# Kernel tuning notes

Measured on AMD Instinct MI355X. Metric: run time of the kernel, lower is better.

The kernel has to match this reference:

```python
import jax, jax.numpy as jnp
import numpy as np
import math

B, T, C = 8, 2048, 1024
N_LAYER, LAYER_ID = 24, 12


def setup_inputs() -> dict:
    key = jax.random.key(0)
    ks = jax.random.split(key, 8)
    # deterministic parameter init, mirroring RWKV_TimeMix.__init__
    ratio_0_to_1 = LAYER_ID / (N_LAYER - 1)
    ratio_1_to_almost0 = 1.0 - LAYER_ID / N_LAYER
    h = np.arange(C, dtype=np.float64)
    time_decay = (-5 + 8 * (h / (C - 1)) ** (0.7 + 1.3 * ratio_0_to_1)).astype(np.float32)
    zigzag = (np.array([(i + 1) % 3 - 1 for i in range(C)], dtype=np.float64) * 0.5)
    time_first = (np.ones(C) * math.log(0.3) + zigzag).astype(np.float32)
    xpos = (np.arange(C, dtype=np.float64) / C)
    time_mix_k = (xpos ** ratio_1_to_almost0).astype(np.float32).reshape(1, 1, C)
    time_mix_v = (xpos ** ratio_1_to_almost0 + 0.3 * ratio_0_to_1).astype(np.float32).reshape(1, 1, C)
    time_mix_r = (xpos ** (0.5 * ratio_1_to_almost0)).astype(np.float32).reshape(1, 1, C)
    scale = 1.0 / math.sqrt(C)
    return {
        "x": jax.random.normal(ks[0], (B, T, C), jnp.float32),
        "time_decay": jnp.asarray(time_decay),
        "time_first": jnp.asarray(time_first),
        "time_mix_k": jnp.asarray(time_mix_k),
        "time_mix_v": jnp.asarray(time_mix_v),
        "time_mix_r": jnp.asarray(time_mix_r),
        "Wk": jax.random.normal(ks[1], (C, C), jnp.float32) * scale,
        "Wv": jax.random.normal(ks[2], (C, C), jnp.float32) * scale,
        "Wr": jax.random.normal(ks[3], (C, C), jnp.float32) * scale,
        "Wo": jax.random.normal(ks[4], (C, C), jnp.float32) * scale,
    }


def wkv_scan(w_decay, u, k, v):
    """Numerically-stable RWKV-4 WKV recurrence.
    w_decay, u: [C]; k, v: [B, T, C]. Returns [B, T, C].
    """
    w = -jnp.exp(w_decay)  # negative decay per channel
    kt = jnp.swapaxes(k, 0, 1)  # [T, B, C]
    vt = jnp.swapaxes(v, 0, 1)
    Bn, Cn = k.shape[0], k.shape[2]
    aa0 = jnp.zeros((Bn, Cn), k.dtype)
    bb0 = jnp.zeros((Bn, Cn), k.dtype)
    pp0 = jnp.full((Bn, Cn), -1e38, k.dtype)

    def step(carry, kv):
        aa, bb, pp = carry
        k_t, v_t = kv
        ww = u + k_t
        q = jnp.maximum(pp, ww)
        e1 = jnp.exp(pp - q)
        e2 = jnp.exp(ww - q)
        y = (e1 * aa + e2 * v_t) / (e1 * bb + e2)
        ww2 = pp + w
        q2 = jnp.maximum(ww2, k_t)
        e1 = jnp.exp(ww2 - q2)
        e2 = jnp.exp(k_t - q2)
        return (e1 * aa + e2 * v_t, e1 * bb + e2, q2), y

    _, ys = jax.lax.scan(step, (aa0, bb0, pp0), (kt, vt))
    return jnp.swapaxes(ys, 0, 1)  # [B, T, C]


def reference(x, time_decay, time_first, time_mix_k, time_mix_v, time_mix_r, Wk, Wv, Wr, Wo):
    # time shift: x_{t-1}, zero at t=0
    xx = jnp.pad(x, ((0, 0), (1, 0), (0, 0)))[:, :-1]
    xk = x * time_mix_k + xx * (1.0 - time_mix_k)
    xv = x * time_mix_v + xx * (1.0 - time_mix_v)
    xr = x * time_mix_r + xx * (1.0 - time_mix_r)
    k = jnp.einsum("btc,oc->bto", xk, Wk)
    v = jnp.einsum("btc,oc->bto", xv, Wv)
    r = jnp.einsum("btc,oc->bto", xr, Wr)
    wkv = wkv_scan(time_decay, time_first, k, v)
    rwkv = jax.nn.sigmoid(r) * wkv
    return jnp.einsum("btc,oc->bto", rwkv, Wo)
```

## Files before the change

kernel.cpp:

```cpp
#include <hip/hip_runtime.h>

#define BB 8
#define TT 2048
#define CC 1024
#define WKV_L 32
#define WKV_NCH (TT / WKV_L)
#define WKV_LOG_NCH 6

typedef __bf16 bf16x8_t __attribute__((ext_vector_type(8)));
typedef float f32x4_t __attribute__((ext_vector_type(4)));
typedef unsigned short ushort8_t __attribute__((ext_vector_type(8)));

__device__ __forceinline__ unsigned short f2bf(float f) {
  unsigned u = __float_as_uint(f);
  u += 0x7fffu + ((u >> 16) & 1u);
  return (unsigned short)(u >> 16);
}
__device__ __forceinline__ float bf2f(unsigned short s) {
  return __uint_as_float(((unsigned)s) << 16);
}

#define GLOAD16(gp, lp)                                                        \
  __builtin_amdgcn_global_load_lds(                                            \
      (const __attribute__((address_space(1))) void*)(gp),                     \
      (__attribute__((address_space(3))) void*)(lp), 16, 0, 0)

#define MIXGRID 2048
#define CASTGRID 256

__global__ __launch_bounds__(256) void mix3_castw_kernel(
    const float* __restrict__ x, const float* __restrict__ tmk,
    const float* __restrict__ tmv, const float* __restrict__ tmr,
    unsigned short* __restrict__ xk, unsigned short* __restrict__ xv,
    unsigned short* __restrict__ xr,
    const float* __restrict__ w0, const float* __restrict__ w1,
    const float* __restrict__ w2, const float* __restrict__ w3,
    unsigned short* __restrict__ o0, unsigned short* __restrict__ o1,
    unsigned short* __restrict__ o2, unsigned short* __restrict__ o3) {
  const int bid = blockIdx.x;
  const int tid = threadIdx.x;
  if (bid < MIXGRID) {
    const size_t total8 = (size_t)BB * TT * CC / 8;
    for (size_t i = (size_t)bid * 256 + tid; i < total8;
         i += (size_t)MIXGRID * 256) {
      size_t e = i * 8;
      int c = (int)(e & (CC - 1));
      int t = (int)((e >> 10) & (TT - 1));
      float4 xa = *(const float4*)(x + e);
      float4 xb = *(const float4*)(x + e + 4);
      float4 pa = make_float4(0.f, 0.f, 0.f, 0.f), pb = pa;
      if (t > 0) {
        pa = *(const float4*)(x + e - CC);
        pb = *(const float4*)(x + e - CC + 4);
      }
      float4 mka = *(const float4*)(tmk + c), mkb = *(const float4*)(tmk + c + 4);
      float4 mva = *(const float4*)(tmv + c), mvb = *(const float4*)(tmv + c + 4);
      float4 mra = *(const float4*)(tmr + c), mrb = *(const float4*)(tmr + c + 4);
      ushort8_t ok, ov, orr;
#define MIX1(dst, idx, xv_, pv_, m_) dst[idx] = f2bf(xv_ * m_ + pv_ * (1.f - m_));
      MIX1(ok, 0, xa.x, pa.x, mka.x) MIX1(ok, 1, xa.y, pa.y, mka.y)
      MIX1(ok, 2, xa.z, pa.z, mka.z) MIX1(ok, 3, xa.w, pa.w, mka.w)
      MIX1(ok, 4, xb.x, pb.x, mkb.x) MIX1(ok, 5, xb.y, pb.y, mkb.y)
      MIX1(ok, 6, xb.z, pb.z, mkb.z) MIX1(ok, 7, xb.w, pb.w, mkb.w)
      MIX1(ov, 0, xa.x, pa.x, mva.x) MIX1(ov, 1, xa.y, pa.y, mva.y)
      MIX1(ov, 2, xa.z, pa.z, mva.z) MIX1(ov, 3, xa.w, pa.w, mva.w)
      MIX1(ov, 4, xb.x, pb.x, mvb.x) MIX1(ov, 5, xb.y, pb.y, mvb.y)
      MIX1(ov, 6, xb.z, pb.z, mvb.z) MIX1(ov, 7, xb.w, pb.w, mvb.w)
      MIX1(orr, 0, xa.x, pa.x, mra.x) MIX1(orr, 1, xa.y, pa.y, mra.y)
      MIX1(orr, 2, xa.z, pa.z, mra.z) MIX1(orr, 3, xa.w, pa.w, mra.w)
      MIX1(orr, 4, xb.x, pb.x, mrb.x) MIX1(orr, 5, xb.y, pb.y, mrb.y)
      MIX1(orr, 6, xb.z, pb.z, mrb.z) MIX1(orr, 7, xb.w, pb.w, mrb.w)
#undef MIX1
      *(ushort8_t*)(xk + e) = ok;
      *(ushort8_t*)(xv + e) = ov;
      *(ushort8_t*)(xr + e) = orr;
    }
  } else {
    const int n4 = CC * CC / 4;
    for (int i = (bid - MIXGRID) * 256 + tid; i < 4 * n4;
         i += CASTGRID * 256) {
      int sel = i / n4;
      int j = i - sel * n4;
      const float* w = sel == 0 ? w0 : sel == 1 ? w1 : sel == 2 ? w2 : w3;
      unsigned short* o = sel == 0 ? o0 : sel == 1 ? o1 : sel == 2 ? o2 : o3;
      float4 v = ((const float4*)w)[j];
      ushort4 u;
      u.x = f2bf(v.x); u.y = f2bf(v.y); u.z = f2bf(v.z); u.w = f2bf(v.w);
      ((ushort4*)o)[j] = u;
    }
  }
}

#define NT8 (CC / 64)

template <typename EPI>
__device__ __forceinline__ void gemm8_body(unsigned short* lds8,
                                           const unsigned short* __restrict__ A,
                                           const unsigned short* __restrict__ Bm,
                                           int tm, int tn, EPI epi) {
  const int tid = threadIdx.x;
  const int lane = tid & 63;
  const int wid = tid >> 6;
  const int wr = wid >> 2;
  const int wc = wid & 3;
  const int fr = lane & 15;
  const int fk = lane >> 4;

  const int srow = tid >> 3;
  const int gcol = (((tid & 7) ^ (srow & 7)) << 3);
  const unsigned short* Ag = A + (size_t)(tm * 256 + srow) * CC + gcol;
  const unsigned short* Bg = Bm + (size_t)(tn * 256 + srow) * CC + gcol;
  const int ldst = tid << 3;

  const int rowA = wr * 16 + fr;
  const int rowB = wc * 16 + fr;
  const int sx0 = ((fk ^ (fr & 7)) << 3);
  const int sx1 = (((4 + fk) ^ (fr & 7)) << 3);

  bf16x8_t aF[4][2];
  bf16x8_t bF[2][2][2];
  f32x4_t acc[8][4] = {};

#define STG_A(T, H)                                                            \
  {                                                                            \
    const unsigned short* g_ = Ag + (size_t)((H) * 128) * CC + (T) * 64;       \
    unsigned short* l_ = &lds8[(((T) & 1) << 14) + (H) * 8192 + ldst];         \
    GLOAD16(g_, l_);                                                           \
    GLOAD16(g_ + (size_t)64 * CC, l_ + 4096);                                  \
  }
#define STG_B(T, H)                                                            \
  {                                                                            \
    const unsigned short* g_ = Bg + (size_t)((H) * 128) * CC + (T) * 64;       \
    unsigned short* l_ = &lds8[32768 + (((T) & 1) << 14) + (H) * 8192 + ldst]; \
    GLOAD16(g_, l_);                                                           \
    GLOAD16(g_ + (size_t)64 * CC, l_ + 4096);                                  \
  }
#define LOADA(MH)                                                              \
  _Pragma("unroll") for (int i_ = 0; i_ < 4; ++i_) {                           \
    aF[i_][0] = *(const bf16x8_t*)&lds8[ab + ((MH) * 4 + i_) * 2048 + sx0];    \
    aF[i_][1] = *(const bf16x8_t*)&lds8[ab + ((MH) * 4 + i_) * 2048 + sx1];    \
  }
#define LOADB(NH)                                                              \
  _Pragma("unroll") for (int j_ = 0; j_ < 2; ++j_) {                           \
    bF[NH][j_][0] = *(const bf16x8_t*)&lds8[bb + ((NH) * 2 + j_) * 4096 + sx0];\
    bF[NH][j_][1] = *(const bf16x8_t*)&lds8[bb + ((NH) * 2 + j_) * 4096 + sx1];\
  }
#define MFMAQ(MH, NH)                                                          \
  _Pragma("unroll") for (int i_ = 0; i_ < 4; ++i_)                             \
  _Pragma("unroll") for (int j_ = 0; j_ < 2; ++j_) {                           \
    acc[(MH) * 4 + i_][(NH) * 2 + j_] = __builtin_amdgcn_mfma_f32_16x16x32_bf16( \
        aF[i_][0], bF[NH][j_][0], acc[(MH) * 4 + i_][(NH) * 2 + j_], 0, 0, 0); \
    acc[(MH) * 4 + i_][(NH) * 2 + j_] = __builtin_amdgcn_mfma_f32_16x16x32_bf16( \
        aF[i_][1], bF[NH][j_][1], acc[(MH) * 4 + i_][(NH) * 2 + j_], 0, 0, 0); \
  }

  STG_A(0, 0) STG_B(0, 0) STG_A(0, 1) STG_B(0, 1)
  STG_A(1, 0) STG_B(1, 0) STG_A(1, 1)
  asm volatile("s_waitcnt vmcnt(10)" ::: "memory");
  __builtin_amdgcn_s_barrier();

#pragma unroll
  for (int t = 0; t < NT8; ++t) {
    const int ab = ((t & 1) << 14) + rowA * 64;
    const int bb = 32768 + ((t & 1) << 14) + rowB * 64;
    LOADA(0) LOADB(0)
    if (t + 1 < NT8) { STG_B(t + 1, 1) }
    asm volatile("s_waitcnt vmcnt(8)" ::: "memory");
    __builtin_amdgcn_s_barrier();
    __builtin_amdgcn_s_setprio(1);
    MFMAQ(0, 0)
    __builtin_amdgcn_s_setprio(0);
    __builtin_amdgcn_s_barrier();
    LOADB(1)
    if (t + 2 < NT8) { STG_A(t + 2, 0) }
    __builtin_amdgcn_s_barrier();
    __builtin_amdgcn_s_setprio(1);
    MFMAQ(0, 1)
    __builtin_amdgcn_s_setprio(0);
    __builtin_amdgcn_s_barrier();
    LOADA(1)
    if (t + 2 < NT8) { STG_B(t + 2, 0) }
    __builtin_amdgcn_s_barrier();
    __builtin_amdgcn_s_setprio(1);
    MFMAQ(1, 0)
    __builtin_amdgcn_s_setprio(0);
    __builtin_amdgcn_s_barrier();
    if (t + 2 < NT8) { STG_A(t + 2, 1) }
    asm volatile("s_waitcnt vmcnt(10)" ::: "memory");
    __builtin_amdgcn_s_barrier();
    __builtin_amdgcn_s_setprio(1);
    MFMAQ(1, 1)
    __builtin_amdgcn_s_setprio(0);
    __builtin_amdgcn_s_barrier();
  }

#pragma unroll
  for (int im = 0; im < 8; ++im)
#pragma unroll
    for (int jn = 0; jn < 4; ++jn)
#pragma unroll
      for (int rg = 0; rg < 4; ++rg)
        epi((size_t)(tm * 256 + wr * 16 + im * 32 + (fk << 2) + rg) * CC +
                (size_t)(tn * 256 + wc * 16 + jn * 64 + fr),
            acc[im][jn][rg]);
#undef STG_A
#undef STG_B
#undef LOADA
#undef LOADB
#undef MFMAQ
}

__global__ __launch_bounds__(512, 2) void gemm8_kvr(
    const unsigned short* __restrict__ xk, const unsigned short* __restrict__ xv,
    const unsigned short* __restrict__ xr, const unsigned short* __restrict__ Wk,
    const unsigned short* __restrict__ Wv, const unsigned short* __restrict__ Wr,
    unsigned short* __restrict__ kout, unsigned short* __restrict__ vout,
    unsigned short* __restrict__ rout) {
  __shared__ unsigned short lds8[65536];
  int orig = blockIdx.x;
  int wg = (orig & 7) * 96 + (orig >> 3);
  int which = wg >> 8;
  int rr = wg & 255;
  int tm = rr >> 2;
  int tn = rr & 3;
  const unsigned short* A = which == 0 ? xk : which == 1 ? xv : xr;
  const unsigned short* Bm = which == 0 ? Wk : which == 1 ? Wv : Wr;
  unsigned short* o = which == 0 ? kout : which == 1 ? vout : rout;
  gemm8_body(lds8, A, Bm, tm, tn,
             [&](size_t off, float val) { o[off] = f2bf(val); });
}

__global__ __launch_bounds__(512, 2) void gemm8_one(const unsigned short* __restrict__ A,
                         const unsigned short* __restrict__ Bm,
                         float* __restrict__ Cm) {
  __shared__ unsigned short lds8[65536];
  int orig = blockIdx.x;
  int wg = (orig & 7) * 32 + (orig >> 3);
  int tm = wg >> 2;
  int tn = wg & 3;
  gemm8_body(lds8, A, Bm, tm, tn,
             [&](size_t off, float val) { Cm[off] = val; });
}

__global__ __launch_bounds__(256) void wkv_phase1(const unsigned short* __restrict__ k,
                           const unsigned short* __restrict__ v,
                           const float* __restrict__ wdec,
                           float* __restrict__ Sa, float* __restrict__ Sb,
                           float* __restrict__ Sp) {
  int idx = blockIdx.x * blockDim.x + threadIdx.x;
  int c = (idx & (CC / 2 - 1)) << 1;
  int bj = idx >> 9;
  int j = bj & (WKV_NCH - 1);
  int b = bj >> WKV_LOG_NCH;
  float w0 = -__expf(wdec[c]), w1 = -__expf(wdec[c + 1]);
  size_t off = ((size_t)b * TT + (size_t)j * WKV_L) * CC + c;
  float aa0 = 0.f, bb0 = 0.f, pp0 = -1e38f;
  float aa1 = 0.f, bb1 = 0.f, pp1 = -1e38f;
  ushort2 kk = *(const ushort2*)(k + off);
  ushort2 vv = *(const ushort2*)(v + off);
  for (int t = 0; t < WKV_L; ++t) {
    size_t noff = off + ((t + 1 < WKV_L) ? CC : 0);
    ushort2 nk = *(const ushort2*)(k + noff);
    ushort2 nv = *(const ushort2*)(v + noff);
    float k0 = bf2f(kk.x), k1 = bf2f(kk.y);
    float v0 = bf2f(vv.x), v1 = bf2f(vv.y);
    pp0 += w0; pp1 += w1;
    float d0 = k0 - pp0, d1 = k1 - pp1;
    if (d0 > 8.f) { float s = __expf(-d0); aa0 *= s; bb0 *= s; pp0 = k0; d0 = 0.f; }
    if (d1 > 8.f) { float s = __expf(-d1); aa1 *= s; bb1 *= s; pp1 = k1; d1 = 0.f; }
    float E0 = __expf(d0), E1 = __expf(d1);
    aa0 = fmaf(E0, v0, aa0); bb0 += E0;
    aa1 = fmaf(E1, v1, aa1); bb1 += E1;
    kk = nk; vv = nv; off = noff;
  }
  size_t s = (size_t)bj * CC + c;
  *(float2*)(Sa + s) = make_float2(aa0, aa1);
  *(float2*)(Sb + s) = make_float2(bb0, bb1);
  *(float2*)(Sp + s) = make_float2(pp0, pp1);
}

__global__ __launch_bounds__(256) void wkv_phase2(const float* __restrict__ wdec,
                           const float* __restrict__ Sa, const float* __restrict__ Sb,
                           const float* __restrict__ Sp,
                           float* __restrict__ Ia, float* __restrict__ Ib,
                           float* __restrict__ Ip) {
  int idx = blockIdx.x * blockDim.x + threadIdx.x;
  if (idx >= BB * CC) return;
  int c = idx & (CC - 1);
  int b = idx >> 10;
  float wL = -__expf(wdec[c]) * (float)WKV_L;
  float aa = 0.f, bb = 0.f, pp = -1e38f;
  for (int j = 0; j < WKV_NCH; ++j) {
    size_t s = (size_t)(b * WKV_NCH + j) * CC + c;
    Ia[s] = aa; Ib[s] = bb; Ip[s] = pp;
    float pd = pp + wL;
    float ps = Sp[s];
    float q = fmaxf(pd, ps);
    float e1 = __expf(pd - q);
    float e2 = __expf(ps - q);
    aa = fmaf(e1, aa, e2 * Sa[s]);
    bb = fmaf(e1, bb, e2 * Sb[s]);
    pp = q;
  }
}

__global__ __launch_bounds__(256) void wkv_phase3(const unsigned short* __restrict__ k,
                           const unsigned short* __restrict__ v,
                           const unsigned short* r,
                           const float* __restrict__ wdec,
                           const float* __restrict__ u,
                           const float* __restrict__ Ia, const float* __restrict__ Ib,
                           const float* __restrict__ Ip,
                           unsigned short* out) {
  int idx = blockIdx.x * blockDim.x + threadIdx.x;
  int c = (idx & (CC / 2 - 1)) << 1;
  int bj = idx >> 9;
  int j = bj & (WKV_NCH - 1);
  int b = bj >> WKV_LOG_NCH;
  float w0 = -__expf(wdec[c]), w1 = -__expf(wdec[c + 1]);
  float u0 = u[c], u1 = u[c + 1];
  size_t st = (size_t)bj * CC + c;
  float2 a2 = *(const float2*)(Ia + st);
  float2 b2 = *(const float2*)(Ib + st);
  float2 p2 = *(const float2*)(Ip + st);
  float aa0 = a2.x, bb0 = b2.x, pp0 = p2.x;
  float aa1 = a2.y, bb1 = b2.y, pp1 = p2.y;
  size_t off = ((size_t)b * TT + (size_t)j * WKV_L) * CC + c;
  ushort2 kk = *(const ushort2*)(k + off);
  ushort2 vv = *(const ushort2*)(v + off);
  ushort2 rr2 = *(const ushort2*)(r + off);
  for (int t = 0; t < WKV_L; ++t) {
    size_t noff = off + ((t + 1 < WKV_L) ? CC : 0);
    ushort2 nk = *(const ushort2*)(k + noff);
    ushort2 nv = *(const ushort2*)(v + noff);
    ushort2 nr = *(const ushort2*)(r + noff);
    float k0 = bf2f(kk.x), k1 = bf2f(kk.y);
    float v0 = bf2f(vv.x), v1 = bf2f(vv.y);
    float dy0 = fminf(u0 + k0 - pp0, 60.f);
    float dy1 = fminf(u1 + k1 - pp1, 60.f);
    float Eu0 = __expf(dy0), Eu1 = __expf(dy1);
    float y0 = fmaf(Eu0, v0, aa0) / (bb0 + Eu0);
    float y1 = fmaf(Eu1, v1, aa1) / (bb1 + Eu1);
    float sr0 = 1.f / (1.f + __expf(-bf2f(rr2.x)));
    float sr1 = 1.f / (1.f + __expf(-bf2f(rr2.y)));
    ushort2 o;
    o.x = f2bf(sr0 * y0);
    o.y = f2bf(sr1 * y1);
    *(ushort2*)(out + off) = o;
    pp0 += w0; pp1 += w1;
    float d0 = k0 - pp0, d1 = k1 - pp1;
    if (d0 > 8.f) { float s = __expf(-d0); aa0 *= s; bb0 *= s; pp0 = k0; d0 = 0.f; }
    if (d1 > 8.f) { float s = __expf(-d1); aa1 *= s; bb1 *= s; pp1 = k1; d1 = 0.f; }
    float E0 = __expf(d0), E1 = __expf(d1);
    aa0 = fmaf(E0, v0, aa0); bb0 += E0;
    aa1 = fmaf(E1, v1, aa1); bb1 += E1;
    kk = nk; vv = nv; rr2 = nr; off = noff;
  }
}

extern "C" void kernel_launch(void* const* d_in, const int* in_sizes, int n_in,
                              void* d_out, int out_size, void* d_ws, size_t ws_size,
                              hipStream_t stream) {
  const float* x    = (const float*)d_in[0];
  const float* tdec = (const float*)d_in[1];
  const float* tfir = (const float*)d_in[2];
  const float* tmk  = (const float*)d_in[3];
  const float* tmv  = (const float*)d_in[4];
  const float* tmr  = (const float*)d_in[5];
  const float* Wk   = (const float*)d_in[6];
  const float* Wv   = (const float*)d_in[7];
  const float* Wr   = (const float*)d_in[8];
  const float* Wo   = (const float*)d_in[9];

  const size_t M = (size_t)BB * TT;
  const size_t mixbytes = M * CC * 2;
  const size_t wbytes = (size_t)CC * CC * 2;
  const size_t nstate = (size_t)BB * WKV_NCH * CC;

  char* ws = (char*)d_ws;
  unsigned short* xkb = (unsigned short*)ws;  ws += mixbytes;
  unsigned short* xvb = (unsigned short*)ws;  ws += mixbytes;
  unsigned short* xrb = (unsigned short*)ws;  ws += mixbytes;
  unsigned short* Wkb = (unsigned short*)ws; ws += wbytes;
  unsigned short* Wvb = (unsigned short*)ws; ws += wbytes;
  unsigned short* Wrb = (unsigned short*)ws; ws += wbytes;
  unsigned short* Wob = (unsigned short*)ws; ws += wbytes;
  unsigned short* kbuf = (unsigned short*)ws; ws += mixbytes;
  unsigned short* vbuf = (unsigned short*)ws; ws += mixbytes;
  unsigned short* rbuf = (unsigned short*)ws; ws += mixbytes;
  char* so = (char*)xkb;
  float* Sa = (float*)so; so += nstate * 4;
  float* Sb = (float*)so; so += nstate * 4;
  float* Sp = (float*)so; so += nstate * 4;
  float* Ia = (float*)so; so += nstate * 4;
  float* Ib = (float*)so; so += nstate * 4;
  float* Ip = (float*)so; so += nstate * 4;

  dim3 blk(256);
  dim3 blk8(512);
  const int wkv_grid = (int)(nstate / 2 / 256);

  mix3_castw_kernel<<<MIXGRID + CASTGRID, blk, 0, stream>>>(
      x, tmk, tmv, tmr, xkb, xvb, xrb,
      Wk, Wv, Wr, Wo, Wkb, Wvb, Wrb, Wob);
  gemm8_kvr<<<768, blk8, 0, stream>>>(xkb, xvb, xrb, Wkb, Wvb, Wrb,
                                      kbuf, vbuf, rbuf);

  wkv_phase1<<<wkv_grid, blk, 0, stream>>>(kbuf, vbuf, tdec, Sa, Sb, Sp);
  wkv_phase2<<<(BB * CC + 255) / 256, blk, 0, stream>>>(tdec, Sa, Sb, Sp, Ia, Ib, Ip);
  wkv_phase3<<<wkv_grid, blk, 0, stream>>>(kbuf, vbuf, rbuf, tdec, tfir,
                                           Ia, Ib, Ip, rbuf);

  gemm8_one<<<256, blk8, 0, stream>>>(rbuf, Wob, (float*)d_out);
}
```

Baseline: 238.8 us.

## Prefetch next-tile LDS fragments before barriers to overlap with MFMA

Restructures the GEMM main loop so the LDS fragment reads for the next quarter (and the next k-tile's first A/B fragments) are issued right after each MFMA block, before the barrier. The aim is to hide LDS read latency behind outstanding MFMA work. The vmcnt waits are retuned to match the shifted load schedule, with special cases for the last iterations. The tighter wait accounting risks races if the counts are off.

```diff
diff --git a/kernel.cpp b/kernel.cpp
--- a/kernel.cpp
+++ b/kernel.cpp
@@ -112,8 +112,8 @@
   const unsigned short* Bg = Bm + (size_t)(tn * 256 + srow) * CC + gcol;
   const int ldst = tid << 3;
 
-  const int rowA = wr * 16 + fr;
-  const int rowB = wc * 16 + fr;
+  const int ab0 = (wr * 16 + fr) * 64;
+  const int bb0 = 32768 + (wc * 16 + fr) * 64;
   const int sx0 = ((fk ^ (fr & 7)) << 3);
   const int sx1 = (((4 + fk) ^ (fr & 7)) << 3);
 
@@ -135,15 +135,15 @@
     GLOAD16(g_, l_);                                                           \
     GLOAD16(g_ + (size_t)64 * CC, l_ + 4096);                                  \
   }
-#define LOADA(MH)                                                              \
+#define LOADA(MH, AB)                                                          \
   _Pragma("unroll") for (int i_ = 0; i_ < 4; ++i_) {                           \
-    aF[i_][0] = *(const bf16x8_t*)&lds8[ab + ((MH) * 4 + i_) * 2048 + sx0];    \
-    aF[i_][1] = *(const bf16x8_t*)&lds8[ab + ((MH) * 4 + i_) * 2048 + sx1];    \
-  }
-#define LOADB(NH)                                                              \
+    aF[i_][0] = *(const bf16x8_t*)&lds8[(AB) + ((MH) * 4 + i_) * 2048 + sx0];  \
+    aF[i_][1] = *(const bf16x8_t*)&lds8[(AB) + ((MH) * 4 + i_) * 2048 + sx1];  \
+  }
+#define LOADB(NH, BB2)                                                         \
   _Pragma("unroll") for (int j_ = 0; j_ < 2; ++j_) {                           \
-    bF[NH][j_][0] = *(const bf16x8_t*)&lds8[bb + ((NH) * 2 + j_) * 4096 + sx0];\
-    bF[NH][j_][1] = *(const bf16x8_t*)&lds8[bb + ((NH) * 2 + j_) * 4096 + sx1];\
+    bF[NH][j_][0] = *(const bf16x8_t*)&lds8[(BB2) + ((NH) * 2 + j_) * 4096 + sx0]; \
+    bF[NH][j_][1] = *(const bf16x8_t*)&lds8[(BB2) + ((NH) * 2 + j_) * 4096 + sx1]; \
   }
 #define MFMAQ(MH, NH)                                                          \
   _Pragma("unroll") for (int i_ = 0; i_ < 4; ++i_)                             \
@@ -156,41 +156,50 @@
 
   STG_A(0, 0) STG_B(0, 0) STG_A(0, 1) STG_B(0, 1)
   STG_A(1, 0) STG_B(1, 0) STG_A(1, 1)
-  asm volatile("s_waitcnt vmcnt(10)" ::: "memory");
+  asm volatile("s_waitcnt vmcnt(6)" ::: "memory");
   __builtin_amdgcn_s_barrier();
+  LOADA(0, ab0) LOADB(0, bb0)
 
 #pragma unroll
   for (int t = 0; t < NT8; ++t) {
-    const int ab = ((t & 1) << 14) + rowA * 64;
-    const int bb = 32768 + ((t & 1) << 14) + rowB * 64;
-    LOADA(0) LOADB(0)
-    if (t + 1 < NT8) { STG_B(t + 1, 1) }
-    asm volatile("s_waitcnt vmcnt(8)" ::: "memory");
+    const int pc = (t & 1) << 14;
+    const int pn = ((t + 1) & 1) << 14;
+    if (t + 1 < NT8) {
+      STG_B(t + 1, 1)
+      asm volatile("s_waitcnt vmcnt(8)" ::: "memory");
+    } else {
+      asm volatile("s_waitcnt vmcnt(0)" ::: "memory");
+    }
     __builtin_amdgcn_s_barrier();
     __builtin_amdgcn_s_setprio(1);
     MFMAQ(0, 0)
     __builtin_amdgcn_s_setprio(0);
-    __builtin_amdgcn_s_barrier();
-    LOADB(1)
+    LOADB(1, bb0 + pc)
+    __builtin_amdgcn_s_barrier();
     if (t + 2 < NT8) { STG_A(t + 2, 0) }
     __builtin_amdgcn_s_barrier();
     __builtin_amdgcn_s_setprio(1);
     MFMAQ(0, 1)
     __builtin_amdgcn_s_setprio(0);
-    __builtin_amdgcn_s_barrier();
-    LOADA(1)
+    LOADA(1, ab0 + pc)
+    __builtin_amdgcn_s_barrier();
     if (t + 2 < NT8) { STG_B(t + 2, 0) }
     __builtin_amdgcn_s_barrier();
     __builtin_amdgcn_s_setprio(1);
     MFMAQ(1, 0)
     __builtin_amdgcn_s_setprio(0);
     __builtin_amdgcn_s_barrier();
-    if (t + 2 < NT8) { STG_A(t + 2, 1) }
-    asm volatile("s_waitcnt vmcnt(10)" ::: "memory");
+    if (t + 2 < NT8) {
+      STG_A(t + 2, 1)
+      asm volatile("s_waitcnt vmcnt(8)" ::: "memory");
+    } else if (t + 1 < NT8) {
+      asm volatile("s_waitcnt vmcnt(2)" ::: "memory");
+    }
     __builtin_amdgcn_s_barrier();
     __builtin_amdgcn_s_setprio(1);
     MFMAQ(1, 1)
     __builtin_amdgcn_s_setprio(0);
+    if (t + 1 < NT8) { LOADA(0, ab0 + pn) LOADB(0, bb0 + pn) }
     __builtin_amdgcn_s_barrier();
   }
 
```

Result: no change. 237.6 us (-0.5%).
